# Kernel tuning notes

Measured on AMD Instinct MI355X. Metric: run time of the kernel, lower is better.

## Reference

```python
import jax, jax.numpy as jnp
import numpy as np

N, FIN, FOUT = 4096, 256, 256


def setup_inputs() -> dict:
    key = jax.random.key(0)
    ks = jax.random.split(key, 6)
    x = jax.random.normal(ks[0], (N, FIN), jnp.float32)
    adj = jax.random.randint(ks[1], (N, N), 0, 2, jnp.int32)  # dense 0/1 adjacency
    W = jax.random.normal(ks[2], (FOUT, FIN), jnp.float32) / np.sqrt(FIN)
    b = jax.random.normal(ks[3], (FOUT,), jnp.float32) * 0.01
    att_w = jax.random.normal(ks[4], (2 * FOUT,), jnp.float32) / np.sqrt(2.0 * FOUT)  # Linear(2F,1).weight squeezed
    att_b = jax.random.normal(ks[5], (), jnp.float32) * 0.01
    return {"x": x, "adj": adj, "W": W, "b": b, "att_w": att_w, "att_b": att_b}


def reference(x, adj, W, b, att_w, att_b):
    n = x.shape[0]
    fo = W.shape[0]
    h = x @ W.T + b  # [N, Fout]
    # score(i,j) = att([h_i ; h_j]) = h_i.w1 + h_j.w2 + att_b  -> no [N,N,2F] concat
    s = (h @ att_w[:fo])[:, None] + (h @ att_w[fo:])[None, :] + att_b  # [N, N]
    edge = adj == 1
    # GLOBAL softmax over all edges (faithful to F.softmax(stacked_scores, dim=0))
    gmax = jnp.max(jnp.where(edge, s, -jnp.inf))
    e = jnp.exp(s - gmax)
    denom = jnp.sum(jnp.where(edge, e, 0.0))
    p = (e / denom).reshape(-1)  # softmaxed score per pair (valid at edges)
    # original indexes attention_scores[j] by NODE id j into the row-major edge list:
    # recover the score of the j-th global edge (j = 0..N-1) via cumsum rank + scatter
    flat = edge.reshape(-1)
    rank = jnp.cumsum(flat.astype(jnp.int32)) - 1  # rank of each edge in row-major order
    idx = jnp.where(flat, rank, n)  # non-edges and ranks >= n get dropped
    w_node = jnp.zeros((n,), h.dtype).at[idx].set(p, mode="drop")  # [N]
    # output[i] = sum_{j: adj[i,j]==1} w_node[j] * h[j]
    out = jax.nn.relu(edge.astype(h.dtype) @ (w_node[:, None] * h))
    return out
```

## Files before the change

### kernel.cpp

```cpp
#include <hip/hip_runtime.h>
#include <cstdint>
#include <cstddef>

#define NN 4096
#define FDIM 256

typedef __attribute__((ext_vector_type(4))) float fx4;
typedef __attribute__((ext_vector_type(8))) short s8v;

__device__ inline uint16_t f2bf(float f) {
    union { float f; uint32_t u; } v; v.f = f;
    const uint32_t u = v.u;
    return (uint16_t)((u + 0x7FFFu + ((u >> 16) & 1u)) >> 16);
}

__global__ __launch_bounds__(512, 4) void k_h(const float* __restrict__ x,
        const float* __restrict__ W, const float* __restrict__ bias,
        const float* __restrict__ att_w, const int* __restrict__ adj,
        uint16_t* __restrict__ gt, uint32_t* __restrict__ bitw,
        float* __restrict__ a1p, float* __restrict__ a2p) {
    __shared__ __align__(16) float xs[2][64 * 68];
    __shared__ __align__(16) float wt[2][64 * 68];
    const int bi = blockIdx.x, bf = blockIdx.y;
    const int t = threadIdx.x;
    const int t256 = t & 255;
    const int kh = t >> 8;
    const int tx = t256 & 15, ty = t256 >> 4;
    const int pr0 = (bi * 4 + bf) * 16;
    float acc[4][4] = {};
    float rx[8], rw[8];
    #pragma unroll
    for (int u = 0; u < 8; ++u) {
        const int e = t + 512 * u, r = e >> 6, c = e & 63;
        rx[u] = x[(size_t)(bi * 64 + r) * 256 + c];
        rw[u] = W[(size_t)(bf * 64 + r) * 256 + c];
    }
    for (int p = 0; p < 4; ++p) {
        float* xb = xs[p & 1];
        float* wb = wt[p & 1];
        #pragma unroll
        for (int u = 0; u < 8; ++u) {
            const int e = t + 512 * u, r = e >> 6, c = e & 63;
            const int sw = 8 * ((c & 7) ^ ((c >> 3) & 7));
            xb[c * 68 + (r ^ sw)] = rx[u];
            wb[c * 68 + (r ^ sw)] = rw[u];
        }
        __syncthreads();
        if (p < 3) {
            const int kc = (p + 1) * 64;
            #pragma unroll
            for (int u = 0; u < 8; ++u) {
                const int e = t + 512 * u, r = e >> 6, c = e & 63;
                rx[u] = x[(size_t)(bi * 64 + r) * 256 + kc + c];
                rw[u] = W[(size_t)(bf * 64 + r) * 256 + kc + c];
            }
        }
        const int wi = p * 512 + t;
        const int prow = pr0 + (wi >> 7), pw = wi & 127;
        int4 pa[8];
        {
            const int* ap = adj + (size_t)prow * NN + pw * 32;
            #pragma unroll
            for (int j = 0; j < 8; ++j) pa[j] = *(const int4*)(ap + j * 4);
        }
        #pragma unroll 8
        for (int k = 0; k < 32; ++k) {
            const int kk = kh * 32 + k;
            const int sw = 8 * ((kk & 7) ^ ((kk >> 3) & 7));
            const fx4 av = *(const fx4*)(xb + kk * 68 + ((ty * 4) ^ sw));
            const fx4 bv = *(const fx4*)(wb + kk * 68 + ((tx * 4) ^ sw));
            #pragma unroll
            for (int u = 0; u < 4; ++u)
                #pragma unroll
                for (int v = 0; v < 4; ++v)
                    acc[u][v] += av[u] * bv[v];
        }
        uint32_t bm = 0;
        #pragma unroll
        for (int j = 0; j < 8; ++j) {
            bm |= (uint32_t)(pa[j].x & 1) << (4 * j);
            bm |= (uint32_t)(pa[j].y & 1) << (4 * j + 1);
            bm |= (uint32_t)(pa[j].z & 1) << (4 * j + 2);
            bm |= (uint32_t)(pa[j].w & 1) << (4 * j + 3);
        }
        bitw[(size_t)prow * 128 + pw] = bm;
    }
    __syncthreads();
    float* cbuf = xs[0];
    if (kh == 1) {
        #pragma unroll
        for (int u = 0; u < 4; ++u)
            *(fx4*)(cbuf + t256 * 16 + u * 4) = *(const fx4*)(&acc[u][0]);
    }
    __syncthreads();
    if (kh == 0) {
        float* tileT = wt[0];
        #pragma unroll
        for (int u = 0; u < 4; ++u) {
            const fx4 o = *(const fx4*)(cbuf + t256 * 16 + u * 4);
            #pragma unroll
            for (int v = 0; v < 4; ++v) acc[u][v] += o[v];
        }
        const fx4 bv = *(const fx4*)(bias + bf * 64 + tx * 4);
        const fx4 w1v = *(const fx4*)(att_w + bf * 64 + tx * 4);
        const fx4 w2v = *(const fx4*)(att_w + 256 + bf * 64 + tx * 4);
        #pragma unroll
        for (int u = 0; u < 4; ++u) {
            const int i = bi * 64 + ty * 4 + u;
            fx4 r;
            float s1 = 0.f, s2 = 0.f;
            #pragma unroll
            for (int v = 0; v < 4; ++v) {
                r[v] = acc[u][v] + bv[v];
                s1 += r[v] * w1v[v];
                s2 += r[v] * w2v[v];
            }
            #pragma unroll
            for (int v = 0; v < 4; ++v)
                tileT[(tx * 4 + v) * 68 + ty * 4 + u] = r[v];
            #pragma unroll
            for (int d = 8; d > 0; d >>= 1) {
                s1 += __shfl_down(s1, d, 16);
                s2 += __shfl_down(s2, d, 16);
            }
            if (tx == 0) {
                a1p[bf * NN + i] = s1;
                a2p[bf * NN + i] = s2;
            }
        }
    }
    __syncthreads();
    {
        const float* tileT = wt[0];
        const int fl = t >> 3, cb = t & 7;
        s8v v;
        #pragma unroll
        for (int lo = 0; lo < 8; ++lo)
            v[lo] = (short)f2bf(tileT[fl * 68 + cb * 8 + lo]);
        *(s8v*)(gt + (size_t)(bf * 64 + fl) * NN + bi * 64 + cb * 8) = v;
    }
}

__global__ __launch_bounds__(1024) void k_prep(const float* __restrict__ a1p,
        const float* __restrict__ a2p, const int* __restrict__ adj,
        float* __restrict__ E1, float* __restrict__ E2,
        uint16_t* __restrict__ wbf, float* __restrict__ Sg) {
    __shared__ float E1s[NN];
    __shared__ float E2s[NN];
    __shared__ float wraw_s[NN];
    __shared__ float red1[16], red2[16];
    __shared__ int wtot[16];
    __shared__ int base_s;
    const int t = threadIdx.x, lane = t & 63, wv = t >> 6;
    fx4 v1 = {0.f, 0.f, 0.f, 0.f}, v2 = {0.f, 0.f, 0.f, 0.f};
    #pragma unroll
    for (int bf = 0; bf < 4; ++bf) {
        v1 += *(const fx4*)(a1p + bf * NN + t * 4);
        v2 += *(const fx4*)(a2p + bf * NN + t * 4);
    }
    float m1 = fmaxf(fmaxf(v1[0], v1[1]), fmaxf(v1[2], v1[3]));
    float m2 = fmaxf(fmaxf(v2[0], v2[1]), fmaxf(v2[2], v2[3]));
    #pragma unroll
    for (int d = 32; d > 0; d >>= 1) {
        m1 = fmaxf(m1, __shfl_down(m1, d));
        m2 = fmaxf(m2, __shfl_down(m2, d));
    }
    if (lane == 0) { red1[wv] = m1; red2[wv] = m2; }
    __syncthreads();
    if (t == 0) {
        float mm1 = -1e30f, mm2 = -1e30f;
        for (int k = 0; k < 16; ++k) {
            mm1 = fmaxf(mm1, red1[k]);
            mm2 = fmaxf(mm2, red2[k]);
        }
        red1[0] = mm1; red2[0] = mm2;
        *Sg = 0.f;
        base_s = 0;
    }
    __syncthreads();
    const float M1 = red1[0], M2 = red2[0];
    fx4 e1v, e2v, z4 = {0.f, 0.f, 0.f, 0.f};
    #pragma unroll
    for (int j = 0; j < 4; ++j) {
        e1v[j] = expf(v1[j] - M1);
        e2v[j] = expf(v2[j] - M2);
    }
    *(fx4*)(E1s + t * 4) = e1v;
    *(fx4*)(E2s + t * 4) = e2v;
    *(fx4*)(E1 + t * 4) = e1v;
    *(fx4*)(E2 + t * 4) = e2v;
    *(fx4*)(wraw_s + t * 4) = z4;
    __syncthreads();
    for (int row = 0; row < NN; ++row) {
        const int base = base_s;
        if (base >= NN) break;
        const int4 a = ((const int4*)(adj + (size_t)row * NN))[t];
        const int vj[4] = {a.x, a.y, a.z, a.w};
        int cnt = 0;
        #pragma unroll
        for (int j = 0; j < 4; ++j) cnt += (vj[j] == 1);
        int inc = cnt;
        #pragma unroll
        for (int d = 1; d < 64; d <<= 1) {
            const int y = __shfl_up(inc, d);
            if (lane >= d) inc += y;
        }
        if (lane == 63) wtot[wv] = inc;
        __syncthreads();
        int wbase = 0, total = 0;
        #pragma unroll
        for (int w = 0; w < 16; ++w) {
            const int xw = wtot[w];
            total += xw;
            wbase += (w < wv) ? xw : 0;
        }
        if (t == 0) base_s = base + total;
        int r = base + wbase + inc - cnt;
        if (cnt && r < NN) {
            const float e1 = E1s[row];
            #pragma unroll
            for (int j = 0; j < 4; ++j) {
                if (vj[j] == 1) {
                    if (r < NN) wraw_s[r] = e1 * E2s[t * 4 + j];
                    ++r;
                }
            }
        }
        __syncthreads();
    }
    __syncthreads();
    {
        const fx4 wv4 = *(const fx4*)(wraw_s + t * 4);
        uint2 o;
        o.x = (uint32_t)f2bf(wv4[0]) | ((uint32_t)f2bf(wv4[1]) << 16);
        o.y = (uint32_t)f2bf(wv4[2]) | ((uint32_t)f2bf(wv4[3]) << 16);
        *(uint2*)(wbf + t * 4) = o;
    }
}

__global__ __launch_bounds__(256, 2) void k_fused(const uint32_t* __restrict__ bitw,
        const uint16_t* __restrict__ gt, const float* __restrict__ E1,
        const float* __restrict__ E2, const uint16_t* __restrict__ wbf,
        uint16_t* __restrict__ part, float* __restrict__ Sg, int krange) {
    __shared__ __align__(16) uint16_t As[2][64 * 72];
    __shared__ float sgred[4];
    const int ib = blockIdx.x, ks = blockIdx.y;
    const int t = threadIdx.x;
    const int wv = t >> 6, lane = t & 63;
    const int q = lane >> 4, m16 = lane & 15;
    const int i0 = ib * 64, k0 = ks * krange;
    const int ksteps = krange >> 6;
    const int srow = t & 63, scg = t >> 6;
    const int sh = (scg & 1) * 16;
    fx4 acc[4][4];
    #pragma unroll
    for (int a = 0; a < 4; ++a)
        #pragma unroll
        for (int b2 = 0; b2 < 4; ++b2) acc[a][b2] = (fx4){0.f, 0.f, 0.f, 0.f};
    float sS = 0.f;
    const float e1row = E1[i0 + srow];
    const uint32_t* brow = bitw + (size_t)(i0 + srow) * 128 + (k0 >> 5) + (scg >> 1);
    const uint16_t* rowp[4];
    #pragma unroll
    for (int ft = 0; ft < 4; ++ft)
        rowp[ft] = gt + (size_t)(wv * 64 + ft * 16 + m16) * NN + q * 8;

    uint32_t bitsC = brow[0];
    uint4 wpC0 = *(const uint4*)(wbf + k0 + scg * 16);
    uint4 wpC1 = *(const uint4*)(wbf + k0 + scg * 16 + 8);
    s8v B0[4][2], B1[4][2];
    #pragma unroll
    for (int ft = 0; ft < 4; ++ft) {
        B0[ft][0] = *(const s8v*)(rowp[ft] + k0);
        B0[ft][1] = *(const s8v*)(rowp[ft] + k0 + 32);
    }

    auto step = [&](s8v (&Bc)[4][2], s8v (&Bn)[4][2], int stp) {
        const int cur = stp & 1;
        const int kk = k0 + stp * 64;
        fx4 e2v[4];
        #pragma unroll
        for (int j = 0; j < 4; ++j)
            e2v[j] = *(const fx4*)(E2 + kk + scg * 16 + j * 4);
        const uint32_t bits = bitsC >> sh;
        uint32_t wpa[8];
        wpa[0] = wpC0.x; wpa[1] = wpC0.y; wpa[2] = wpC0.z; wpa[3] = wpC0.w;
        wpa[4] = wpC1.x; wpa[5] = wpC1.y; wpa[6] = wpC1.z; wpa[7] = wpC1.w;
        float s16 = 0.f;
        uint32_t ob[8];
        #pragma unroll
        for (int pp = 0; pp < 8; ++pp) {
            const uint32_t b0 = (bits >> (2 * pp)) & 1u;
            const uint32_t b1 = (bits >> (2 * pp + 1)) & 1u;
            ob[pp] = wpa[pp] & ((b0 ? 0xFFFFu : 0u) | (b1 ? 0xFFFF0000u : 0u));
            s16 += (b0 ? e2v[pp >> 1][(pp & 1) * 2] : 0.f) +
                   (b1 ? e2v[pp >> 1][(pp & 1) * 2 + 1] : 0.f);
        }
        sS += e1row * s16;
        uint16_t* dstAs = &As[cur][srow * 72 + scg * 16];
        *(uint2*)(dstAs + 0)  = make_uint2(ob[0], ob[1]);
        *(uint2*)(dstAs + 4)  = make_uint2(ob[2], ob[3]);
        *(uint2*)(dstAs + 8)  = make_uint2(ob[4], ob[5]);
        *(uint2*)(dstAs + 12) = make_uint2(ob[6], ob[7]);
        __syncthreads();
        if (stp + 1 < ksteps) {
            bitsC = brow[(stp + 1) * 2];
            wpC0 = *(const uint4*)(wbf + kk + 64 + scg * 16);
            wpC1 = *(const uint4*)(wbf + kk + 64 + scg * 16 + 8);
            #pragma unroll
            for (int ft = 0; ft < 4; ++ft) {
                Bn[ft][0] = *(const s8v*)(rowp[ft] + kk + 64);
                Bn[ft][1] = *(const s8v*)(rowp[ft] + kk + 64 + 32);
            }
        }
        s8v afr[4][2];
        #pragma unroll
        for (int it = 0; it < 4; ++it)
            #pragma unroll
            for (int khh = 0; khh < 2; ++khh)
                afr[it][khh] = *(const s8v*)(&As[cur][(it * 16 + m16) * 72 +
                                                      khh * 32 + q * 8]);
        #pragma unroll
        for (int ft = 0; ft < 4; ++ft)
            #pragma unroll
            for (int khh = 0; khh < 2; ++khh)
                #pragma unroll
                for (int it = 0; it < 4; ++it)
                    acc[it][ft] = __builtin_amdgcn_mfma_f32_16x16x32_bf16(
                        afr[it][khh], Bc[ft][khh], acc[it][ft], 0, 0, 0);
    };

    for (int stp = 0; stp < ksteps; stp += 2) {
        step(B0, B1, stp);
        step(B1, B0, stp + 1);
    }

    #pragma unroll
    for (int d = 32; d > 0; d >>= 1) sS += __shfl_down(sS, d);
    if (lane == 0) sgred[wv] = sS;
    __syncthreads();
    if (t == 0)
        atomicAdd(Sg, sgred[0] + sgred[1] + sgred[2] + sgred[3]);
    uint16_t* dst = part + (size_t)ks * NN * FDIM;
    #pragma unroll
    for (int it = 0; it < 4; ++it) {
        #pragma unroll
        for (int ft = 0; ft < 4; ++ft) {
            const int f = wv * 64 + ft * 16 + m16;
            #pragma unroll
            for (int r = 0; r < 4; ++r) {
                const int i = i0 + it * 16 + q * 4 + r;
                dst[(size_t)i * FDIM + f] = f2bf(acc[it][ft][r]);
            }
        }
    }
}

__global__ __launch_bounds__(256) void k_out(const uint16_t* __restrict__ part,
        const float* __restrict__ Sg, float* __restrict__ out, int nsplit) {
    const size_t idx = ((size_t)blockIdx.x * 256 + threadIdx.x) * 8;
    const float inv = 1.0f / (*Sg);
    float s[8] = {};
    for (int k = 0; k < nsplit; ++k) {
        const s8v v = *(const s8v*)(part + (size_t)k * NN * FDIM + idx);
        #pragma unroll
        for (int j = 0; j < 8; ++j) {
            union { uint32_t u; float f; } cv;
            cv.u = ((uint32_t)(uint16_t)v[j]) << 16;
            s[j] += cv.f;
        }
    }
    fx4 r0, r1;
    #pragma unroll
    for (int j = 0; j < 4; ++j) {
        r0[j] = fmaxf(s[j], 0.f) * inv;
        r1[j] = fmaxf(s[4 + j], 0.f) * inv;
    }
    *(fx4*)(out + idx) = r0;
    *(fx4*)(out + idx + 4) = r1;
}

extern "C" void kernel_launch(void* const* d_in, const int* in_sizes, int n_in,
                              void* d_out, int out_size, void* d_ws, size_t ws_size,
                              hipStream_t stream) {
    const float* x     = (const float*)d_in[0];
    const int*   adj   = (const int*)d_in[1];
    const float* W     = (const float*)d_in[2];
    const float* bias  = (const float*)d_in[3];
    const float* att_w = (const float*)d_in[4];
    float* out = (float*)d_out;
    char* ws = (char*)d_ws;
    uint16_t* gt   = (uint16_t*)(ws + 0);
    uint32_t* bitw = (uint32_t*)(ws + 2097152);
    float*    a1p  = (float*)(ws + 4194304);
    float*    a2p  = (float*)(ws + 4259840);
    float*    E1   = (float*)(ws + 4325376);
    float*    E2   = (float*)(ws + 4341760);
    uint16_t* wbf  = (uint16_t*)(ws + 4358144);
    float*    Sg   = (float*)(ws + 4366336);
    uint16_t* part = (uint16_t*)(ws + 4366592);
    (void)in_sizes; (void)n_in; (void)out_size;

    const size_t avail = (ws_size > 4366592) ? (ws_size - 4366592) : 0;
    int splitk = 1;
    while (splitk < 8 &&
           (size_t)(splitk * 2) * NN * FDIM * sizeof(uint16_t) <= avail)
        splitk <<= 1;
    const int krange = NN / splitk;

    k_h    <<<dim3(64, 4), 512, 0, stream>>>(x, W, bias, att_w, adj, gt, bitw, a1p, a2p);
    k_prep <<<dim3(1), 1024, 0, stream>>>(a1p, a2p, adj, E1, E2, wbf, Sg);
    k_fused<<<dim3(64, splitk), 256, 0, stream>>>(bitw, gt, E1, E2, wbf, part, Sg, krange);
    k_out  <<<dim3(512), 256, 0, stream>>>(part, Sg, out, splitk);
}
```

Baseline: 155.7 us.

## Build masked A fragments in registers instead of staging through LDS

The fused kernel no longer writes the masked weight tile into shared memory and synchronizes each k-step. Each lane now loads the adjacency bits and bf16 weights for its own MFMA fragment and masks them directly in registers. The global softmax denominator partial is computed only by wave 0 and added with an atomic, so the block-level reduction goes away. In exchange, all four waves redundantly load and mask the same bits and weights, and the explicit register double-buffering of B with prefetch is dropped, which may expose global-load latency.

After: 161.4 us. 1.04x slower.

```diff
diff --git a/kernel.cpp b/kernel.cpp
--- a/kernel.cpp
+++ b/kernel.cpp
@@ -4,6 +4,7 @@
 
 #define NN 4096
 #define FDIM 256
+#define SPLITK 8
 
 typedef __attribute__((ext_vector_type(4))) float fx4;
 typedef __attribute__((ext_vector_type(8))) short s8v;
@@ -238,109 +239,92 @@
     }
 }
 
-__global__ __launch_bounds__(256, 2) void k_fused(const uint32_t* __restrict__ bitw,
+__global__ __launch_bounds__(256) void k_fused(const uint32_t* __restrict__ bitw,
         const uint16_t* __restrict__ gt, const float* __restrict__ E1,
         const float* __restrict__ E2, const uint16_t* __restrict__ wbf,
         uint16_t* __restrict__ part, float* __restrict__ Sg, int krange) {
-    __shared__ __align__(16) uint16_t As[2][64 * 72];
-    __shared__ float sgred[4];
     const int ib = blockIdx.x, ks = blockIdx.y;
     const int t = threadIdx.x;
     const int wv = t >> 6, lane = t & 63;
     const int q = lane >> 4, m16 = lane & 15;
     const int i0 = ib * 64, k0 = ks * krange;
     const int ksteps = krange >> 6;
-    const int srow = t & 63, scg = t >> 6;
-    const int sh = (scg & 1) * 16;
     fx4 acc[4][4];
     #pragma unroll
     for (int a = 0; a < 4; ++a)
         #pragma unroll
         for (int b2 = 0; b2 < 4; ++b2) acc[a][b2] = (fx4){0.f, 0.f, 0.f, 0.f};
     float sS = 0.f;
-    const float e1row = E1[i0 + srow];
-    const uint32_t* brow = bitw + (size_t)(i0 + srow) * 128 + (k0 >> 5) + (scg >> 1);
+    float e1r[4];
+    #pragma unroll
+    for (int p = 0; p < 4; ++p) e1r[p] = E1[i0 + p * 16 + m16];
     const uint16_t* rowp[4];
     #pragma unroll
     for (int ft = 0; ft < 4; ++ft)
         rowp[ft] = gt + (size_t)(wv * 64 + ft * 16 + m16) * NN + q * 8;
-
-    uint32_t bitsC = brow[0];
-    uint4 wpC0 = *(const uint4*)(wbf + k0 + scg * 16);
-    uint4 wpC1 = *(const uint4*)(wbf + k0 + scg * 16 + 8);
-    s8v B0[4][2], B1[4][2];
-    #pragma unroll
-    for (int ft = 0; ft < 4; ++ft) {
-        B0[ft][0] = *(const s8v*)(rowp[ft] + k0);
-        B0[ft][1] = *(const s8v*)(rowp[ft] + k0 + 32);
-    }
-
-    auto step = [&](s8v (&Bc)[4][2], s8v (&Bn)[4][2], int stp) {
-        const int cur = stp & 1;
+    const uint32_t* bp[4];
+    #pragma unroll
+    for (int it = 0; it < 4; ++it)
+        bp[it] = bitw + (size_t)(i0 + it * 16 + m16) * 128 + (k0 >> 5);
+
+    for (int stp = 0; stp < ksteps; ++stp) {
         const int kk = k0 + stp * 64;
-        fx4 e2v[4];
-        #pragma unroll
-        for (int j = 0; j < 4; ++j)
-            e2v[j] = *(const fx4*)(E2 + kk + scg * 16 + j * 4);
-        const uint32_t bits = bitsC >> sh;
-        uint32_t wpa[8];
-        wpa[0] = wpC0.x; wpa[1] = wpC0.y; wpa[2] = wpC0.z; wpa[3] = wpC0.w;
-        wpa[4] = wpC1.x; wpa[5] = wpC1.y; wpa[6] = wpC1.z; wpa[7] = wpC1.w;
-        float s16 = 0.f;
-        uint32_t ob[8];
-        #pragma unroll
-        for (int pp = 0; pp < 8; ++pp) {
-            const uint32_t b0 = (bits >> (2 * pp)) & 1u;
-            const uint32_t b1 = (bits >> (2 * pp + 1)) & 1u;
-            ob[pp] = wpa[pp] & ((b0 ? 0xFFFFu : 0u) | (b1 ? 0xFFFF0000u : 0u));
-            s16 += (b0 ? e2v[pp >> 1][(pp & 1) * 2] : 0.f) +
-                   (b1 ? e2v[pp >> 1][(pp & 1) * 2 + 1] : 0.f);
-        }
-        sS += e1row * s16;
-        uint16_t* dstAs = &As[cur][srow * 72 + scg * 16];
-        *(uint2*)(dstAs + 0)  = make_uint2(ob[0], ob[1]);
-        *(uint2*)(dstAs + 4)  = make_uint2(ob[2], ob[3]);
-        *(uint2*)(dstAs + 8)  = make_uint2(ob[4], ob[5]);
-        *(uint2*)(dstAs + 12) = make_uint2(ob[6], ob[7]);
-        __syncthreads();
-        if (stp + 1 < ksteps) {
-            bitsC = brow[(stp + 1) * 2];
-            wpC0 = *(const uint4*)(wbf + kk + 64 + scg * 16);
-            wpC1 = *(const uint4*)(wbf + kk + 64 + scg * 16 + 8);
-            #pragma unroll
-            for (int ft = 0; ft < 4; ++ft) {
-                Bn[ft][0] = *(const s8v*)(rowp[ft] + kk + 64);
-                Bn[ft][1] = *(const s8v*)(rowp[ft] + kk + 64 + 32);
-            }
-        }
-        s8v afr[4][2];
-        #pragma unroll
-        for (int it = 0; it < 4; ++it)
+        uint2 bw[4];
+        #pragma unroll
+        for (int it = 0; it < 4; ++it) bw[it] = *(const uint2*)(bp[it] + stp * 2);
+        uint4 wp[2];
+        #pragma unroll
+        for (int khh = 0; khh < 2; ++khh)
+            wp[khh] = *(const uint4*)(wbf + kk + khh * 32 + q * 8);
+        s8v B[4][2];
+        #pragma unroll
+        for (int ft = 0; ft < 4; ++ft)
             #pragma unroll
             for (int khh = 0; khh < 2; ++khh)
-                afr[it][khh] = *(const s8v*)(&As[cur][(it * 16 + m16) * 72 +
-                                                      khh * 32 + q * 8]);
-        #pragma unroll
-        for (int ft = 0; ft < 4; ++ft)
-            #pragma unroll
-            for (int khh = 0; khh < 2; ++khh)
+                B[ft][khh] = *(const s8v*)(rowp[ft] + kk + khh * 32);
+        #pragma unroll
+        for (int it = 0; it < 4; ++it) {
+            #pragma unroll
+            for (int khh = 0; khh < 2; ++khh) {
+                const uint32_t b8 = ((khh ? bw[it].y : bw[it].x) >> (q * 8)) & 0xFFu;
+                union { uint32_t w[4]; s8v v; } af;
+                const uint32_t* wpw = (const uint32_t*)&wp[khh];
                 #pragma unroll
-                for (int it = 0; it < 4; ++it)
+                for (int n = 0; n < 4; ++n) {
+                    const uint32_t msk = ((b8 >> (2 * n)) & 1u ? 0xFFFFu : 0u) |
+                                         ((b8 >> (2 * n + 1)) & 1u ? 0xFFFF0000u : 0u);
+                    af.w[n] = wpw[n] & msk;
+                }
+                #pragma unroll
+                for (int ft = 0; ft < 4; ++ft)
                     acc[it][ft] = __builtin_amdgcn_mfma_f32_16x16x32_bf16(
-                        afr[it][khh], Bc[ft][khh], acc[it][ft], 0, 0, 0);
-    };
-
-    for (int stp = 0; stp < ksteps; stp += 2) {
-        step(B0, B1, stp);
-        step(B1, B0, stp + 1);
-    }
-
-    #pragma unroll
-    for (int d = 32; d > 0; d >>= 1) sS += __shfl_down(sS, d);
-    if (lane == 0) sgred[wv] = sS;
-    __syncthreads();
-    if (t == 0)
-        atomicAdd(Sg, sgred[0] + sgred[1] + sgred[2] + sgred[3]);
+                        af.v, B[ft][khh], acc[it][ft], 0, 0, 0);
+            }
+        }
+        if (wv == 0) {
+            #pragma unroll
+            for (int khh = 0; khh < 2; ++khh) {
+                const fx4 e2a = *(const fx4*)(E2 + kk + khh * 32 + q * 8);
+                const fx4 e2b = *(const fx4*)(E2 + kk + khh * 32 + q * 8 + 4);
+                #pragma unroll
+                for (int it = 0; it < 4; ++it) {
+                    const uint32_t b8 = ((khh ? bw[it].y : bw[it].x) >> (q * 8)) & 0xFFu;
+                    float s8 = 0.f;
+                    #pragma unroll
+                    for (int j = 0; j < 4; ++j) {
+                        s8 += ((b8 >> j) & 1u) ? e2a[j] : 0.f;
+                        s8 += ((b8 >> (j + 4)) & 1u) ? e2b[j] : 0.f;
+                    }
+                    sS += e1r[it] * s8;
+                }
+            }
+        }
+    }
+    if (wv == 0) {
+        #pragma unroll
+        for (int d = 32; d > 0; d >>= 1) sS += __shfl_down(sS, d);
+        if (lane == 0) atomicAdd(Sg, sS);
+    }
     uint16_t* dst = part + (size_t)ks * NN * FDIM;
     #pragma unroll
     for (int it = 0; it < 4; ++it) {
```
